# Optimization experiments

Hardware: AMD Instinct MI355X
Metric: run time of the kernel (lower is better)

## Reference

```python
import jax, jax.numpy as jnp
import numpy as np

OUT = 7  # out_size


def setup_inputs() -> dict:
    key = jax.random.key(0)
    kx, k1, k2, k3, k4 = jax.random.split(key, 5)
    B, C, H, W, Q = 4, 256, 128, 128, 100
    x = jax.random.normal(kx, (B, C, H, W), dtype=jnp.float32)
    # valid boxes: start in [0, W/2), extent in [8, W/2) -> always in-bounds, nonempty
    x1 = jax.random.randint(k1, (B, Q), 0, W // 2)
    y1 = jax.random.randint(k2, (B, Q), 0, H // 2)
    x2 = x1 + jax.random.randint(k3, (B, Q), 8, W // 2)
    y2 = y1 + jax.random.randint(k4, (B, Q), 8, H // 2)
    bidx = jnp.broadcast_to(jnp.arange(B, dtype=jnp.int32)[:, None], (B, Q))
    rois = jnp.stack([bidx, x1, y1, x2, y2], axis=-1).astype(jnp.int32)
    return {"x": x, "rois": rois}


def _bin_edges(start, length, nbins):
    # adaptive_avg_pool2d bin boundaries for bin k over a region of given length:
    #   lo_k = floor(k*L/n), hi_k = ceil((k+1)*L/n)
    # start, length: [B,Q] int; returns (starts, ends) each [B,Q,nbins]
    k = jnp.arange(nbins)
    lo = start[..., None] + (k * length[..., None]) // nbins
    hi = start[..., None] - ((-(k + 1) * length[..., None]) // nbins)  # ceil div
    return lo, hi


def reference(x, rois):
    # x: [B,C,H,W] float, rois: [B,Q,5] int (batch_idx, x1, y1, x2, y2)
    B, C, H, W = x.shape
    Q = rois.shape[1]
    oh = ow = OUT
    # Summed-area table S[b, y, x, c] = sum of x over rows < y, cols < x.
    xc = jnp.moveaxis(x, 1, -1)                       # [B,H,W,C]
    S = jnp.cumsum(jnp.cumsum(xc, axis=1), axis=2)
    S = jnp.pad(S, ((0, 0), (1, 0), (1, 0), (0, 0)))  # [B,H+1,W+1,C]

    x1, y1, x2, y2 = rois[..., 1], rois[..., 2], rois[..., 3], rois[..., 4]
    ys, ye = _bin_edges(y1, y2 - y1, oh)              # [B,Q,oh]
    xs, xe = _bin_edges(x1, x2 - x1, ow)              # [B,Q,ow]

    b = jnp.arange(B)[:, None, None, None]            # [B,1,1,1]
    Ys, Ye = ys[:, :, :, None], ye[:, :, :, None]     # [B,Q,oh,1]
    Xs, Xe = xs[:, :, None, :], xe[:, :, None, :]     # [B,Q,1,ow]

    # rectangle sums per bin via SAT corner differences -> [B,Q,oh,ow,C]
    sums = S[b, Ye, Xe] - S[b, Ys, Xe] - S[b, Ye, Xs] + S[b, Ys, Xs]
    area = ((Ye - Ys) * (Xe - Xs)).astype(x.dtype)[..., None]
    out = sums / area                                  # bin averages

    out = jnp.moveaxis(out, -1, 2)                     # [B,Q,C,oh,ow]
    return out.reshape(B, Q * C, oh, ow)               # cat ROIs along channel dim
```

## Files before the change

### kernel.cpp

```cpp
#include <hip/hip_runtime.h>

#define B_ 4
#define C_ 256
#define H_ 128
#define W_ 128
#define Q_ 100
#define WP_ 132

__global__ __launch_bounds__(512, 4) void roipool_kernel(const float4* __restrict__ x4,
                                                         const int* __restrict__ rois,
                                                         float* __restrict__ out) {
    __shared__ float sat[H_ * WP_];
    __shared__ float qt[4][W_];

    const int c   = blockIdx.x & 255;
    const int b   = blockIdx.x >> 8;
    const int tid = threadIdx.x;

    const float4* src = x4 + (size_t)(b * C_ + c) * (H_ * W_ / 4);
    float4* s4 = (float4*)sat;
    #pragma unroll
    for (int i = 0; i < 8; ++i) {
        int idx  = i * 512 + tid;
        int row  = idx >> 5;
        int col4 = idx & 31;
        s4[row * (WP_ / 4) + col4] = src[idx];
    }
    __syncthreads();

    const int wave = tid >> 6, lane = tid & 63;
    for (int r = wave; r < H_; r += 8) {
        float2* p2 = (float2*)(sat + r * WP_);
        float2 v = p2[lane];
        float s  = v.x + v.y;
        #pragma unroll
        for (int d = 1; d < 64; d <<= 1) {
            float t = __shfl_up(s, d);
            if (lane >= d) s += t;
        }
        float excl = s - (v.x + v.y);
        p2[lane] = make_float2(excl + v.x, excl + v.x + v.y);
    }
    __syncthreads();

    {
        const int qy = tid >> 7;
        const int x  = tid & 127;
        float acc = 0.f;
        #pragma unroll
        for (int j = 0; j < 32; ++j) {
            const int y = qy * 32 + j;
            acc += sat[y * WP_ + x];
            sat[y * WP_ + x] = acc;
        }
        qt[qy][x] = acc;
    }
    __syncthreads();

    if (tid < W_) {
        const int x = tid;
        float t0 = qt[0][x], t1 = qt[1][x], t2 = qt[2][x];
        qt[1][x] = t0;
        qt[2][x] = t0 + t1;
        qt[3][x] = t0 + t1 + t2;
    }
    __syncthreads();

    #pragma unroll
    for (int j = 0; j < 24; ++j) {
        const int e = j * 512 + tid;
        const int y = 32 + (e >> 7);
        const int x = e & 127;
        sat[y * WP_ + x] += qt[y >> 5][x];
    }
    __syncthreads();

    const int* rb = rois + (size_t)b * Q_ * 5;
    for (int t = tid; t < Q_ * 49; t += 512) {
        const int q   = t / 49;
        const int bin = t - q * 49;
        const int oy  = bin / 7;
        const int ox  = bin - oy * 7;

        const int x1 = rb[q * 5 + 1];
        const int y1 = rb[q * 5 + 2];
        const int Lx = rb[q * 5 + 3] - x1;
        const int Ly = rb[q * 5 + 4] - y1;

        const int ys = y1 + (oy * Ly) / 7;
        const int ye = y1 + ((oy + 1) * Ly + 6) / 7;
        const int xs = x1 + (ox * Lx) / 7;
        const int xe = x1 + ((ox + 1) * Lx + 6) / 7;

        const float s11 = sat[(ye - 1) * WP_ + (xe - 1)];
        const float s01 = (ys > 0) ? sat[(ys - 1) * WP_ + (xe - 1)] : 0.f;
        const float s10 = (xs > 0) ? sat[(ye - 1) * WP_ + (xs - 1)] : 0.f;
        const float s00 = (ys > 0 && xs > 0) ? sat[(ys - 1) * WP_ + (xs - 1)] : 0.f;

        const float area = (float)((ye - ys) * (xe - xs));
        out[(((size_t)(b * Q_ + q)) * C_ + c) * 49 + bin] =
            (s11 - s01 - s10 + s00) / area;
    }
}

extern "C" void kernel_launch(void* const* d_in, const int* in_sizes, int n_in,
                              void* d_out, int out_size, void* d_ws, size_t ws_size,
                              hipStream_t stream) {
    const float* x    = (const float*)d_in[0];
    const int*   rois = (const int*)d_in[1];
    float*       outp = (float*)d_out;

    roipool_kernel<<<B_ * C_, 512, 0, stream>>>((const float4*)x, rois, outp);
}
```

Measured before the change: 118.8 us.

## Fuse load with row scan, precompute packed bin edges, vectorize column scan

The horizontal prefix scan now runs in registers straight after the global load, using a 32-lane shuffle scan on float4s, which removes a separate LDS pass and one barrier. ROI bin edges are computed once per (roi,k) and packed into bytes in shared memory instead of being recomputed per bin. The vertical scan uses float4 accesses over 16 row-chunks with a two-level offset pass. The division becomes a hardware reciprocal multiply, which may differ slightly from exact division in rounding.

After: 108.1 us. 9.0% less time.

```diff
diff --git a/kernel.cpp b/kernel.cpp
--- a/kernel.cpp
+++ b/kernel.cpp
@@ -10,96 +10,118 @@
 __global__ __launch_bounds__(512, 4) void roipool_kernel(const float4* __restrict__ x4,
                                                          const int* __restrict__ rois,
                                                          float* __restrict__ out) {
-    __shared__ float sat[H_ * WP_];
-    __shared__ float qt[4][W_];
+    __shared__ __align__(16) float sat[H_ * WP_];
+    __shared__ float4 ot4[16 * 33];
+    __shared__ unsigned int ebl[Q_ * 7];
 
     const int c   = blockIdx.x & 255;
     const int b   = blockIdx.x >> 8;
     const int tid = threadIdx.x;
 
     const float4* src = x4 + (size_t)(b * C_ + c) * (H_ * W_ / 4);
-    float4* s4 = (float4*)sat;
+    const int wv = tid >> 6, ln = tid & 63;
+    const int xl = ln & 31;
     #pragma unroll
     for (int i = 0; i < 8; ++i) {
-        int idx  = i * 512 + tid;
-        int row  = idx >> 5;
-        int col4 = idx & 31;
-        s4[row * (WP_ / 4) + col4] = src[idx];
+        const int r = wv * 16 + i * 2 + (ln >> 5);
+        float4 v = src[wv * 512 + i * 64 + ln];
+        float s = v.x + v.y + v.z + v.w;
+        float run = s;
+        #pragma unroll
+        for (int d = 1; d < 32; d <<= 1) {
+            float t = __shfl_up(run, d);
+            if (xl >= d) run += t;
+        }
+        const float excl = run - s;
+        float4 o;
+        o.x = excl + v.x;
+        o.y = o.x + v.y;
+        o.z = o.y + v.z;
+        o.w = o.z + v.w;
+        ((float4*)(sat + r * WP_))[xl] = o;
     }
-    __syncthreads();
 
-    const int wave = tid >> 6, lane = tid & 63;
-    for (int r = wave; r < H_; r += 8) {
-        float2* p2 = (float2*)(sat + r * WP_);
-        float2 v = p2[lane];
-        float s  = v.x + v.y;
-        #pragma unroll
-        for (int d = 1; d < 64; d <<= 1) {
-            float t = __shfl_up(s, d);
-            if (lane >= d) s += t;
-        }
-        float excl = s - (v.x + v.y);
-        p2[lane] = make_float2(excl + v.x, excl + v.x + v.y);
+    const int* rbase = rois + (size_t)b * Q_ * 5;
+    for (int t = tid; t < Q_ * 7; t += 512) {
+        const int q = t / 7;
+        const int k = t - q * 7;
+        const int* rb = rbase + q * 5;
+        const int x1 = rb[1], y1 = rb[2];
+        const int Lx = rb[3] - x1, Ly = rb[4] - y1;
+        const unsigned int ys = y1 + (k * Ly) / 7;
+        const unsigned int ye = y1 + ((k + 1) * Ly + 6) / 7;
+        const unsigned int xs = x1 + (k * Lx) / 7;
+        const unsigned int xe = x1 + ((k + 1) * Lx + 6) / 7;
+        ebl[t] = ys | (ye << 8) | (xs << 16) | (xe << 24);
     }
     __syncthreads();
 
     {
-        const int qy = tid >> 7;
-        const int x  = tid & 127;
-        float acc = 0.f;
+        float4* s4 = (float4*)sat;
+        const int oct = tid >> 5;
+        const int stp = tid & 31;
+        float4 acc = make_float4(0.f, 0.f, 0.f, 0.f);
         #pragma unroll
-        for (int j = 0; j < 32; ++j) {
-            const int y = qy * 32 + j;
-            acc += sat[y * WP_ + x];
-            sat[y * WP_ + x] = acc;
+        for (int j = 0; j < 8; ++j) {
+            const int y = oct * 8 + j;
+            float4 v = s4[y * 33 + stp];
+            acc.x += v.x; acc.y += v.y; acc.z += v.z; acc.w += v.w;
+            s4[y * 33 + stp] = acc;
         }
-        qt[qy][x] = acc;
+        ot4[oct * 33 + stp] = acc;
     }
     __syncthreads();
 
-    if (tid < W_) {
-        const int x = tid;
-        float t0 = qt[0][x], t1 = qt[1][x], t2 = qt[2][x];
-        qt[1][x] = t0;
-        qt[2][x] = t0 + t1;
-        qt[3][x] = t0 + t1 + t2;
+    if (tid < 32) {
+        float4 run = make_float4(0.f, 0.f, 0.f, 0.f);
+        #pragma unroll
+        for (int k = 0; k < 16; ++k) {
+            float4 v = ot4[k * 33 + tid];
+            ot4[k * 33 + tid] = run;
+            run.x += v.x; run.y += v.y; run.z += v.z; run.w += v.w;
+        }
     }
     __syncthreads();
 
-    #pragma unroll
-    for (int j = 0; j < 24; ++j) {
-        const int e = j * 512 + tid;
-        const int y = 32 + (e >> 7);
-        const int x = e & 127;
-        sat[y * WP_ + x] += qt[y >> 5][x];
+    {
+        float4* s4 = (float4*)sat;
+        #pragma unroll
+        for (int j = 0; j < 8; ++j) {
+            const int f = j * 512 + tid;
+            const int y = f >> 5;
+            const int oc = y >> 3;
+            const int st = f & 31;
+            if (oc > 0) {
+                float4 off = ot4[oc * 33 + st];
+                float4 v = s4[y * 33 + st];
+                v.x += off.x; v.y += off.y; v.z += off.z; v.w += off.w;
+                s4[y * 33 + st] = v;
+            }
+        }
     }
     __syncthreads();
 
-    const int* rb = rois + (size_t)b * Q_ * 5;
+    float* ob = out + (size_t)(b * Q_) * (C_ * 49) + (size_t)c * 49;
     for (int t = tid; t < Q_ * 49; t += 512) {
         const int q   = t / 49;
         const int bin = t - q * 49;
         const int oy  = bin / 7;
         const int ox  = bin - oy * 7;
 
-        const int x1 = rb[q * 5 + 1];
-        const int y1 = rb[q * 5 + 2];
-        const int Lx = rb[q * 5 + 3] - x1;
-        const int Ly = rb[q * 5 + 4] - y1;
-
-        const int ys = y1 + (oy * Ly) / 7;
-        const int ye = y1 + ((oy + 1) * Ly + 6) / 7;
-        const int xs = x1 + (ox * Lx) / 7;
-        const int xe = x1 + ((ox + 1) * Lx + 6) / 7;
+        const unsigned int ey = ebl[q * 7 + oy];
+        const unsigned int ex = ebl[q * 7 + ox];
+        const int ys = ey & 255;
+        const int ye = (ey >> 8) & 255;
+        const int xs = (ex >> 16) & 255;
+        const int xe = ex >> 24;
 
         const float s11 = sat[(ye - 1) * WP_ + (xe - 1)];
         const float s01 = (ys > 0) ? sat[(ys - 1) * WP_ + (xe - 1)] : 0.f;
         const float s10 = (xs > 0) ? sat[(ye - 1) * WP_ + (xs - 1)] : 0.f;
         const float s00 = (ys > 0 && xs > 0) ? sat[(ys - 1) * WP_ + (xs - 1)] : 0.f;
 
-        const float area = (float)((ye - ys) * (xe - xs));
-        out[(((size_t)(b * Q_ + q)) * C_ + c) * 49 + bin] =
-            (s11 - s01 - s10 + s00) / area;
+        const float inv = __builtin_amdgcn_rcpf((float)((ye - ys) * (xe - xs)));
+        ob[(size_t)q * (C_ * 49) + bin] = (s11 - s01 - s10 + s00) * inv;
     }
 }
 
```
